# Kernel tuning notes

Measured on AMD Instinct MI355X. Metric: run time of the kernel, lower is better.

Reference implementation:

```python
import jax, jax.numpy as jnp
import numpy as np


def setup_inputs() -> dict:
    key = jax.random.key(0)
    k1, k2, k3, k4 = jax.random.split(key, 4)
    B, N, C_IN, C_OUT, K = 8, 4096, 64, 64, 16
    H = W = 64  # H * W == N
    x = jax.random.normal(k1, (B, N, C_IN), dtype=jnp.float32)
    edge_index = jax.random.randint(k2, (B, N, K), 0, N, dtype=jnp.int64)
    # 1x1 Conv2d(2*C_IN -> C_OUT) is a [C_OUT, 2*C_IN] matmul + bias
    weight = jax.random.normal(k3, (C_OUT, 2 * C_IN), dtype=jnp.float32) * 0.05
    bias = jax.random.normal(k4, (C_OUT,), dtype=jnp.float32) * 0.01
    return {"x": x, "edge_index": edge_index, "weight": weight, "bias": bias,
            "H": H, "W": W}


def reference(x, edge_index, weight, bias, H, W):
    # x: [B, N, C], edge_index: [B, N, K] with values in [0, N)
    B, N, C = x.shape
    K = edge_index.shape[-1]
    # Gather neighbor features per batch element (batched index_select)
    idx = edge_index.reshape(B, N * K, 1)                      # [B, N*K, 1]
    neighbors = jnp.take_along_axis(x, idx, axis=1)            # [B, N*K, C]
    neighbors = neighbors.reshape(B, N, K, C)                  # [B, N, K, C]
    x_central = x[:, :, None, :]                               # [B, N, 1, C]
    # edge feature: concat([x_i, x_j - x_i]) -> [B, N, K, 2C]
    edge_feat = jnp.concatenate(
        [jnp.broadcast_to(x_central, (B, N, K, C)), neighbors - x_central],
        axis=-1)
    # 1x1 conv + ReLU
    out = jax.nn.relu(jnp.einsum('bnkc,oc->bnko', edge_feat, weight) + bias)
    # max over neighbors k -> [B, N, C_out]
    out = jnp.max(out, axis=2)
    # [B, C_out, N] -> [B, C_out, H, W]
    return jnp.transpose(out, (0, 2, 1)).reshape(B, weight.shape[0], H, W)
```

## Files before the change

### kernel.cpp

```cpp
#include <hip/hip_runtime.h>
#include <stdint.h>

#define B_SZ    8
#define N_PTS   4096
#define C_IN    64
#define C_OUT   64
#define KNN     16
#define ROWS    (B_SZ * N_PTS)

typedef __attribute__((ext_vector_type(8))) short v8s;
typedef __attribute__((ext_vector_type(4))) float v4f;

__device__ inline unsigned short f2bf(float f) {
    unsigned int u = __float_as_uint(f);
    return (unsigned short)((u + 0x7FFFu + ((u >> 16) & 1u)) >> 16);
}

__device__ inline v8s pack8(float4 q0, float4 q1) {
    v8s a;
    a[0] = (short)f2bf(q0.x); a[1] = (short)f2bf(q0.y);
    a[2] = (short)f2bf(q0.z); a[3] = (short)f2bf(q0.w);
    a[4] = (short)f2bf(q1.x); a[5] = (short)f2bf(q1.y);
    a[6] = (short)f2bf(q1.z); a[7] = (short)f2bf(q1.w);
    return a;
}

#define PITCH 68

__global__ __launch_bounds__(256) void wprep_kernel(const float* __restrict__ w,
                                                    v8s* __restrict__ wfrag)
{
    __shared__ float wl[2 * C_IN * C_OUT];
    const int t = threadIdx.x;
    {
        const float4* src = (const float4*)w;
        float4*       dst = (float4*)wl;
#pragma unroll
        for (int i = 0; i < 8; ++i)
            dst[i * 256 + t] = src[i * 256 + t];
    }
    __syncthreads();

    const int tid  = blockIdx.x * 256 + t;
    const int lane = tid & 63;
    const int ks   = (tid >> 6) & 1;
    const int ct   = tid >> 7;
    const int col  = ct * 16 + (lane & 15);
    const int kb   = ks * 32 + 8 * (lane >> 4);

    v8s f;
#pragma unroll
    for (int j = 0; j < 8; ++j) {
        const int k = kb + j;
        const float v = (col < 64)
            ? (wl[col * 128 + k] - wl[col * 128 + 64 + k])
            : wl[(col - 64) * 128 + 64 + k];
        f[j] = (short)f2bf(v);
    }
    wfrag[tid] = f;
}

__global__ __launch_bounds__(256, 2) void proj_nbuf(
    const float* __restrict__ x,
    const v8s*  __restrict__ wfrag,
    unsigned short* __restrict__ nbuf)
{
    const int lane  = threadIdx.x & 63;
    const int wv    = threadIdx.x >> 6;
    const int batch = blockIdx.x & 7;
    const int chunk = blockIdx.x >> 3;
    const int r0    = batch * N_PTS + chunk * 64 + wv * 16;

    v8s bfrag[4][2];
#pragma unroll
    for (int ct = 0; ct < 4; ++ct)
#pragma unroll
        for (int ks = 0; ks < 2; ++ks)
            bfrag[ct][ks] = wfrag[((4 + ct) * 2 + ks) * 64 + lane];

    const int arow = r0 + (lane & 15);
    const int koff = 8 * (lane >> 4);
    v8s afrag[2];
#pragma unroll
    for (int ks = 0; ks < 2; ++ks) {
        const float* xp = x + (size_t)arow * C_IN + ks * 32 + koff;
        afrag[ks] = pack8(*(const float4*)xp, *(const float4*)(xp + 4));
    }

    v4f acc[4];
#pragma unroll
    for (int ct = 0; ct < 4; ++ct)
        acc[ct] = (v4f){0.f, 0.f, 0.f, 0.f};

#pragma unroll
    for (int ks = 0; ks < 2; ++ks)
#pragma unroll
        for (int ct = 0; ct < 4; ++ct)
            acc[ct] = __builtin_amdgcn_mfma_f32_16x16x32_bf16(
                afrag[ks], bfrag[ct][ks], acc[ct], 0, 0, 0);

    const int crow0 = r0 + (lane >> 4) * 4;
    const int ccol  = lane & 15;
#pragma unroll
    for (int ct = 0; ct < 4; ++ct)
#pragma unroll
        for (int reg = 0; reg < 4; ++reg)
            nbuf[(size_t)(crow0 + reg) * C_OUT + ct * 16 + ccol] =
                f2bf(acc[ct][reg]);
}

__global__ __launch_bounds__(256, 4) void gather_fused(
    const float* __restrict__ x,
    const v8s*  __restrict__ wfrag,
    const float* __restrict__ bias,
    const int* __restrict__ eidx,
    const unsigned short* __restrict__ nbuf,
    float* __restrict__ out)
{
    __shared__ float sm[32][PITCH];

    const int t    = threadIdx.x;
    const int lane = t & 63;
    const int wv   = t >> 6;
    const int b    = blockIdx.x & 7;
    const int tn   = blockIdx.x >> 3;
    const int n0   = tn * 32;
    const int r0g  = b * N_PTS + n0;

    int pidx[2];
#pragma unroll
    for (int i = 0; i < 2; ++i)
        pidx[i] = eidx[(size_t)(r0g + wv * 8 + i * 4) * KNN + lane];

    const int rq  = wv & 1;
    const int ch  = wv >> 1;
    v8s bfrag[2][2];
#pragma unroll
    for (int ct = 0; ct < 2; ++ct)
#pragma unroll
        for (int ks = 0; ks < 2; ++ks)
            bfrag[ct][ks] = wfrag[((ch * 2 + ct) * 2 + ks) * 64 + lane];

    {
        const float4* xsrc = (const float4*)(x + (size_t)r0g * C_IN);
#pragma unroll
        for (int i = 0; i < 2; ++i) {
            const int idx = i * 256 + t;
            *(float4*)&sm[idx >> 4][(idx & 15) * 4] = xsrc[idx];
        }
    }
    __syncthreads();

    const int rl0  = rq * 16;
    const int rl   = rl0 + (lane & 15);
    const int koff = 8 * (lane >> 4);
    v8s afrag[2];
#pragma unroll
    for (int ks = 0; ks < 2; ++ks) {
        const float* xp = &sm[rl][ks * 32 + koff];
        afrag[ks] = pack8(*(const float4*)xp, *(const float4*)(xp + 4));
    }

    v4f acc[2];
#pragma unroll
    for (int ct = 0; ct < 2; ++ct) {
        const float bv = bias[ch * 32 + ct * 16 + (lane & 15)];
        acc[ct] = (v4f){bv, bv, bv, bv};
    }
#pragma unroll
    for (int ks = 0; ks < 2; ++ks)
#pragma unroll
        for (int ct = 0; ct < 2; ++ct)
            acc[ct] = __builtin_amdgcn_mfma_f32_16x16x32_bf16(
                afrag[ks], bfrag[ct][ks], acc[ct], 0, 0, 0);

    __syncthreads();

    const int orow = rl0 + (lane >> 4) * 4;
    const int ccol = lane & 15;
#pragma unroll
    for (int ct = 0; ct < 2; ++ct)
#pragma unroll
        for (int reg = 0; reg < 4; ++reg)
            sm[orow + reg][ch * 32 + ct * 16 + ccol] = acc[ct][reg];

    __syncthreads();

    const unsigned short* nb = nbuf + (size_t)b * N_PTS * C_OUT;
    const int o4  = (lane & 15) * 4;
    const int sub = lane >> 4;

#pragma unroll
    for (int i = 0; i < 2; ++i) {
        const int rbl   = wv * 8 + i * 4;
        const int myidx = pidx[i] & (N_PTS - 1);

        const float4 cv = *(const float4*)&sm[rbl + sub][o4];

        float m0 = -1e30f, m1 = -1e30f, m2 = -1e30f, m3 = -1e30f;
#pragma unroll
        for (int k = 0; k < KNN; ++k) {
            const int idx = __shfl(myidx, (lane & 48) | k);
            const uint2 v = *(const uint2*)(nb + (size_t)idx * C_OUT + o4);
            m0 = fmaxf(m0, __uint_as_float(v.x << 16));
            m1 = fmaxf(m1, __uint_as_float(v.x & 0xffff0000u));
            m2 = fmaxf(m2, __uint_as_float(v.y << 16));
            m3 = fmaxf(m3, __uint_as_float(v.y & 0xffff0000u));
        }

        const int nl = rbl + sub;
        sm[nl][o4 + 0] = fmaxf(cv.x + m0, 0.f);
        sm[nl][o4 + 1] = fmaxf(cv.y + m1, 0.f);
        sm[nl][o4 + 2] = fmaxf(cv.z + m2, 0.f);
        sm[nl][o4 + 3] = fmaxf(cv.w + m3, 0.f);
    }

    __syncthreads();

    float* ob = out + (size_t)b * C_OUT * N_PTS + n0;
    const int nn = lane & 31;
    const int oh = lane >> 5;
#pragma unroll
    for (int j = 0; j < 8; ++j) {
        const int o = wv * 16 + j * 2 + oh;
        ob[(size_t)o * N_PTS + nn] = sm[nn][o];
    }
}

extern "C" void kernel_launch(void* const* d_in, const int* in_sizes, int n_in,
                              void* d_out, int out_size, void* d_ws, size_t ws_size,
                              hipStream_t stream)
{
    const float* x    = (const float*)d_in[0];
    const int*   eidx = (const int*)d_in[1];
    const float* w    = (const float*)d_in[2];
    const float* bias = (const float*)d_in[3];
    float*       out  = (float*)d_out;

    unsigned short* nbuf  = (unsigned short*)d_ws;
    v8s*            wfrag = (v8s*)((char*)d_ws + (size_t)ROWS * C_OUT * 2);

    wprep_kernel<<<4, 256, 0, stream>>>(w, wfrag);
    proj_nbuf<<<ROWS / 64, 256, 0, stream>>>(x, wfrag, nbuf);
    gather_fused<<<ROWS / 32, 256, 0, stream>>>(x, wfrag, bias, eidx, nbuf, out);
}
```

Before: 20.55 us.

## Fuse neighbor projection into gather kernel, recomputing per-edge MFMA instead of nbuf

Removes the separate projection kernel and its bf16 intermediate buffer. The fused kernel gathers raw fp32 neighbour rows of x, projects them with MFMA using the neighbour weight fragments, and max-reduces across the 16 neighbours with cross-lane shuffles. This saves a launch and the intermediate write/read. In exchange it does redundant per-edge matmul work and gathers twice as many bytes per neighbour.

```diff
diff --git a/kernel.cpp b/kernel.cpp
--- a/kernel.cpp
+++ b/kernel.cpp
@@ -60,61 +60,11 @@
     wfrag[tid] = f;
 }
 
-__global__ __launch_bounds__(256, 2) void proj_nbuf(
-    const float* __restrict__ x,
-    const v8s*  __restrict__ wfrag,
-    unsigned short* __restrict__ nbuf)
-{
-    const int lane  = threadIdx.x & 63;
-    const int wv    = threadIdx.x >> 6;
-    const int batch = blockIdx.x & 7;
-    const int chunk = blockIdx.x >> 3;
-    const int r0    = batch * N_PTS + chunk * 64 + wv * 16;
-
-    v8s bfrag[4][2];
-#pragma unroll
-    for (int ct = 0; ct < 4; ++ct)
-#pragma unroll
-        for (int ks = 0; ks < 2; ++ks)
-            bfrag[ct][ks] = wfrag[((4 + ct) * 2 + ks) * 64 + lane];
-
-    const int arow = r0 + (lane & 15);
-    const int koff = 8 * (lane >> 4);
-    v8s afrag[2];
-#pragma unroll
-    for (int ks = 0; ks < 2; ++ks) {
-        const float* xp = x + (size_t)arow * C_IN + ks * 32 + koff;
-        afrag[ks] = pack8(*(const float4*)xp, *(const float4*)(xp + 4));
-    }
-
-    v4f acc[4];
-#pragma unroll
-    for (int ct = 0; ct < 4; ++ct)
-        acc[ct] = (v4f){0.f, 0.f, 0.f, 0.f};
-
-#pragma unroll
-    for (int ks = 0; ks < 2; ++ks)
-#pragma unroll
-        for (int ct = 0; ct < 4; ++ct)
-            acc[ct] = __builtin_amdgcn_mfma_f32_16x16x32_bf16(
-                afrag[ks], bfrag[ct][ks], acc[ct], 0, 0, 0);
-
-    const int crow0 = r0 + (lane >> 4) * 4;
-    const int ccol  = lane & 15;
-#pragma unroll
-    for (int ct = 0; ct < 4; ++ct)
-#pragma unroll
-        for (int reg = 0; reg < 4; ++reg)
-            nbuf[(size_t)(crow0 + reg) * C_OUT + ct * 16 + ccol] =
-                f2bf(acc[ct][reg]);
-}
-
-__global__ __launch_bounds__(256, 4) void gather_fused(
+__global__ __launch_bounds__(256, 4) void fused_kernel(
     const float* __restrict__ x,
     const v8s*  __restrict__ wfrag,
     const float* __restrict__ bias,
     const int* __restrict__ eidx,
-    const unsigned short* __restrict__ nbuf,
     float* __restrict__ out)
 {
     __shared__ float sm[32][PITCH];
@@ -127,19 +77,18 @@
     const int n0   = tn * 32;
     const int r0g  = b * N_PTS + n0;
 
-    int pidx[2];
-#pragma unroll
-    for (int i = 0; i < 2; ++i)
-        pidx[i] = eidx[(size_t)(r0g + wv * 8 + i * 4) * KNN + lane];
-
-    const int rq  = wv & 1;
-    const int ch  = wv >> 1;
-    v8s bfrag[2][2];
+    const size_t ebase = (size_t)(r0g + wv * 8) * KNN;
+    int pa = eidx[ebase + lane]      & (N_PTS - 1);
+    int pb = eidx[ebase + 64 + lane] & (N_PTS - 1);
+
+    const int rq = wv & 1, ch = wv >> 1;
+    const int rl0 = rq * 16;
+    v8s bC[2][2];
 #pragma unroll
     for (int ct = 0; ct < 2; ++ct)
 #pragma unroll
         for (int ks = 0; ks < 2; ++ks)
-            bfrag[ct][ks] = wfrag[((ch * 2 + ct) * 2 + ks) * 64 + lane];
+            bC[ct][ks] = wfrag[((ch * 2 + ct) * 2 + ks) * 64 + lane];
 
     {
         const float4* xsrc = (const float4*)(x + (size_t)r0g * C_IN);
@@ -151,14 +100,13 @@
     }
     __syncthreads();
 
-    const int rl0  = rq * 16;
     const int rl   = rl0 + (lane & 15);
     const int koff = 8 * (lane >> 4);
-    v8s afrag[2];
+    v8s af[2];
 #pragma unroll
     for (int ks = 0; ks < 2; ++ks) {
         const float* xp = &sm[rl][ks * 32 + koff];
-        afrag[ks] = pack8(*(const float4*)xp, *(const float4*)(xp + 4));
+        af[ks] = pack8(*(const float4*)xp, *(const float4*)(xp + 4));
     }
 
     v4f acc[2];
@@ -172,49 +120,67 @@
 #pragma unroll
         for (int ct = 0; ct < 2; ++ct)
             acc[ct] = __builtin_amdgcn_mfma_f32_16x16x32_bf16(
-                afrag[ks], bfrag[ct][ks], acc[ct], 0, 0, 0);
-
-    __syncthreads();
-
-    const int orow = rl0 + (lane >> 4) * 4;
-    const int ccol = lane & 15;
-#pragma unroll
-    for (int ct = 0; ct < 2; ++ct)
-#pragma unroll
-        for (int reg = 0; reg < 4; ++reg)
-            sm[orow + reg][ch * 32 + ct * 16 + ccol] = acc[ct][reg];
-
-    __syncthreads();
-
-    const unsigned short* nb = nbuf + (size_t)b * N_PTS * C_OUT;
-    const int o4  = (lane & 15) * 4;
-    const int sub = lane >> 4;
-
-#pragma unroll
-    for (int i = 0; i < 2; ++i) {
-        const int rbl   = wv * 8 + i * 4;
-        const int myidx = pidx[i] & (N_PTS - 1);
-
-        const float4 cv = *(const float4*)&sm[rbl + sub][o4];
-
-        float m0 = -1e30f, m1 = -1e30f, m2 = -1e30f, m3 = -1e30f;
-#pragma unroll
-        for (int k = 0; k < KNN; ++k) {
-            const int idx = __shfl(myidx, (lane & 48) | k);
-            const uint2 v = *(const uint2*)(nb + (size_t)idx * C_OUT + o4);
-            m0 = fmaxf(m0, __uint_as_float(v.x << 16));
-            m1 = fmaxf(m1, __uint_as_float(v.x & 0xffff0000u));
-            m2 = fmaxf(m2, __uint_as_float(v.y << 16));
-            m3 = fmaxf(m3, __uint_as_float(v.y & 0xffff0000u));
+                af[ks], bC[ct][ks], acc[ct], 0, 0, 0);
+
+    v8s bN[4][2];
+#pragma unroll
+    for (int ct = 0; ct < 4; ++ct)
+#pragma unroll
+        for (int ks = 0; ks < 2; ++ks)
+            bN[ct][ks] = wfrag[((4 + ct) * 2 + ks) * 64 + lane];
+
+    __syncthreads();
+
+    {
+        const int orow = rl0 + (lane >> 4) * 4;
+        const int ccol = lane & 15;
+#pragma unroll
+        for (int ct = 0; ct < 2; ++ct)
+#pragma unroll
+            for (int reg = 0; reg < 4; ++reg)
+                sm[orow + reg][ch * 32 + ct * 16 + ccol] = acc[ct][reg];
+    }
+    __syncthreads();
+
+    const float* xb = x + (size_t)b * N_PTS * C_IN;
+    const int g4 = lane >> 4;
+
+#pragma unroll
+    for (int q = 0; q < 8; ++q) {
+        const int src  = (q < 4) ? pa : pb;
+        const int idxn = __shfl(src, ((q & 3) << 4) | (lane & 15));
+
+        const float* gp = xb + (size_t)idxn * C_IN + koff;
+        const v8s A0 = pack8(*(const float4*)gp,        *(const float4*)(gp + 4));
+        const v8s A1 = pack8(*(const float4*)(gp + 32), *(const float4*)(gp + 36));
+
+        v4f pc[4];
+#pragma unroll
+        for (int ct = 0; ct < 4; ++ct)
+            pc[ct] = (v4f){0.f, 0.f, 0.f, 0.f};
+#pragma unroll
+        for (int ct = 0; ct < 4; ++ct) {
+            pc[ct] = __builtin_amdgcn_mfma_f32_16x16x32_bf16(A0, bN[ct][0], pc[ct], 0, 0, 0);
+            pc[ct] = __builtin_amdgcn_mfma_f32_16x16x32_bf16(A1, bN[ct][1], pc[ct], 0, 0, 0);
         }
 
-        const int nl = rbl + sub;
-        sm[nl][o4 + 0] = fmaxf(cv.x + m0, 0.f);
-        sm[nl][o4 + 1] = fmaxf(cv.y + m1, 0.f);
-        sm[nl][o4 + 2] = fmaxf(cv.z + m2, 0.f);
-        sm[nl][o4 + 3] = fmaxf(cv.w + m3, 0.f);
-    }
-
+        float m[4];
+#pragma unroll
+        for (int ct = 0; ct < 4; ++ct) {
+            float r = fmaxf(fmaxf(pc[ct][0], pc[ct][1]),
+                            fmaxf(pc[ct][2], pc[ct][3]));
+            r = fmaxf(r, __shfl_xor(r, 16));
+            r = fmaxf(r, __shfl_xor(r, 32));
+            m[ct] = r;
+        }
+        const float msel = (g4 == 0) ? m[0] : (g4 == 1) ? m[1]
+                         : (g4 == 2) ? m[2] : m[3];
+
+        const int nl = wv * 8 + q;
+        const int oc = g4 * 16 + (lane & 15);
+        const float cv = sm[nl][oc];
+        sm[nl][oc] = fmaxf(cv + msel, 0.f);
+    }
     __syncthreads();
 
     float* ob = out + (size_t)b * C_OUT * N_PTS + n0;
@@ -237,10 +203,8 @@
     const float* bias = (const float*)d_in[3];
     float*       out  = (float*)d_out;
 
-    unsigned short* nbuf  = (unsigned short*)d_ws;
-    v8s*            wfrag = (v8s*)((char*)d_ws + (size_t)ROWS * C_OUT * 2);
+    v8s* wfrag = (v8s*)d_ws;
 
     wprep_kernel<<<4, 256, 0, stream>>>(w, wfrag);
-    proj_nbuf<<<ROWS / 64, 256, 0, stream>>>(x, wfrag, nbuf);
-    gather_fused<<<ROWS / 32, 256, 0, stream>>>(x, wfrag, bias, eidx, nbuf, out);
-}
+    fused_kernel<<<ROWS / 32, 256, 0, stream>>>(x, wfrag, bias, eidx, out);
+}
```

Result: slower. 28.99 us (+41.1%).
